# Kernel tuning notes

Measured on AMD Instinct MI355X. Metric: run time of the kernel, lower is better.

Reference implementation:

```python
import jax, jax.numpy as jnp
import numpy as np

N = 8192          # mesh vertices
E = 49152         # directed edges (avg degree 6)
M = 25            # kernel_size per pseudo-dim
DIM = 3           # pseudo-coordinate dim
K = M ** DIM      # 15625 weight matrices per layer
S = 2 ** DIM      # 8 nonzero degree-1 B-spline products per edge
LC, UC = -0.22703196, 0.36853024   # curvature range
LM, UM = 1.2585511, 1.648841       # myelin range
R = 10.0
LAYER_DIMS = [(2, 32), (32, 64), (64, 64), (64, 32), (32, 1)]


def transform(x):
    # rescale curv/myelin channels into [-R, R] with clamping (matches torch masking)
    t0 = (x[:, 0] - LC) / (UC - LC) * (2.0 * R) - R
    t1 = (x[:, 1] - LM) / (UM - LM) * (2.0 * R) - R
    return jnp.stack([jnp.clip(t0, -R, R), jnp.clip(t1, -R, R)], axis=1)


def spline_basis(pseudo):
    # open B-spline, degree 1: v in [0, M-1); 8 corner products per edge
    v = pseudo * (M - 1)
    lo = jnp.floor(v)
    f = v - lo                                                    # [E, DIM]
    lo = lo.astype(jnp.int32)
    bits = (jnp.arange(S)[:, None] >> jnp.arange(DIM)[None, :]) & 1   # [S, DIM]
    oh = bits.astype(pseudo.dtype)
    basis = jnp.prod(oh[None] * f[:, None, :] + (1.0 - oh[None]) * (1.0 - f[:, None, :]), axis=-1)  # [E, S]
    strides = (M ** jnp.arange(DIM)).astype(jnp.int32)
    wi = jnp.sum((lo[:, None, :] + bits[None]) * strides[None, None, :], axis=-1)  # [E, S] kernel indices
    return basis, wi


def spline_conv(h, src, dst, basis, wi, W, root, bias):
    xj = h[src]                                             # [E, Fin] gather
    msg = jnp.zeros((xj.shape[0], W.shape[2]), h.dtype)
    for s in range(S):                                      # fixed 8-way basis loop
        msg = msg + basis[:, s, None] * jnp.einsum('ei,eio->eo', xj, W[wi[:, s]])
    agg = jax.ops.segment_sum(msg, dst, num_segments=N)     # scatter-sum (norm=False)
    return agg + h @ root + bias


def setup_inputs() -> dict:
    key = jax.random.key(0)
    ks = jax.random.split(key, 3 + 2 * len(LAYER_DIMS))
    inp = {
        "x": jax.random.normal(ks[0], (N, 2), dtype=jnp.float32),
        "edge_index": jax.random.randint(ks[1], (2, E), 0, N),
        "pseudo": jax.random.uniform(ks[2], (E, DIM), dtype=jnp.float32),
    }
    for i, (fi, fo) in enumerate(LAYER_DIMS):
        kw, kr = ks[3 + 2 * i], ks[4 + 2 * i]
        inp[f"W{i+1}"] = jax.random.normal(kw, (K, fi, fo), dtype=jnp.float32) / np.float32(np.sqrt(fi * S))
        inp[f"root{i+1}"] = jax.random.normal(kr, (fi, fo), dtype=jnp.float32) / np.float32(np.sqrt(fi))
        inp[f"b{i+1}"] = jnp.zeros((fo,), dtype=jnp.float32)
    return inp


def reference(x, edge_index, pseudo, W1, root1, b1, W2, root2, b2, W3, root3, b3,
              W4, root4, b4, W5, root5, b5):
    src, dst = edge_index[0], edge_index[1]
    basis, wi = spline_basis(pseudo)   # shared across all 5 layers, as in the torch model
    h = transform(x)
    for W, r, b in ((W1, root1, b1), (W2, root2, b2), (W3, root3, b3),
                    (W4, root4, b4), (W5, root5, b5)):
        h = jax.nn.elu(spline_conv(h, src, dst, basis, wi, W, r, b))
    return h.reshape(-1)
```

## Files before the change

### kernel.cpp

```cpp
#include <hip/hip_runtime.h>
#include <math.h>

#define NV 8192
#define EV 49152
#define KK 15625

__device__ __forceinline__ void edge_frac(const float* __restrict__ pseudo, int e,
                                          float f[3], int lo[3]) {
#pragma unroll
    for (int j = 0; j < 3; ++j) {
        float v = pseudo[e * 3 + j] * 24.0f;
        float fl = floorf(v);
        int l = (int)fl;
        l = l < 0 ? 0 : (l > 23 ? 23 : l);
        lo[j] = l;
        f[j] = v - (float)l;
    }
}

__global__ void transform_kernel(const float* __restrict__ x, float* __restrict__ h0) {
    int n = blockIdx.x * blockDim.x + threadIdx.x;
    if (n >= NV) return;
    const float LC = -0.22703196f, UC = 0.36853024f;
    const float LM = 1.2585511f, UM = 1.648841f;
    const float R = 10.0f;
    float t0 = (x[n * 2 + 0] - LC) / (UC - LC) * (2.0f * R) - R;
    float t1 = (x[n * 2 + 1] - LM) / (UM - LM) * (2.0f * R) - R;
    h0[n * 2 + 0] = fminf(fmaxf(t0, -R), R);
    h0[n * 2 + 1] = fminf(fmaxf(t1, -R), R);
}

__global__ void hist_kernel(const float* __restrict__ pseudo, int* __restrict__ counts) {
    int e = blockIdx.x * blockDim.x + threadIdx.x;
    if (e >= EV) return;
    float f[3]; int lo[3];
    edge_frac(pseudo, e, f, lo);
#pragma unroll
    for (int s = 0; s < 8; ++s) {
        int wi = (lo[0] + (s & 1)) + 25 * (lo[1] + ((s >> 1) & 1)) + 625 * (lo[2] + ((s >> 2) & 1));
        atomicAdd(&counts[wi], 1);
    }
}

__global__ void scan_kernel(const int* __restrict__ counts, int* __restrict__ offsets,
                            int* __restrict__ cursor) {
    __shared__ int sums[256];
    const int CH = 62;
    int t = threadIdx.x;
    int base = t * CH;
    int s = 0;
    for (int i = 0; i < CH; ++i) {
        int idx = base + i;
        if (idx < KK) s += counts[idx];
    }
    sums[t] = s;
    __syncthreads();
    for (int d = 1; d < 256; d <<= 1) {
        int v = (t >= d) ? sums[t - d] : 0;
        __syncthreads();
        sums[t] += v;
        __syncthreads();
    }
    int run = (t > 0) ? sums[t - 1] : 0;
    for (int i = 0; i < CH; ++i) {
        int idx = base + i;
        if (idx < KK) {
            offsets[idx] = run;
            cursor[idx] = run;
            run += counts[idx];
        }
    }
    if (t == 255) offsets[KK] = run;
}

__global__ void scatter_kernel(const float* __restrict__ pseudo, const int* __restrict__ ei,
                               int* __restrict__ cursor,
                               int2* __restrict__ pair_sb, int* __restrict__ pair_dst) {
    int e = blockIdx.x * blockDim.x + threadIdx.x;
    if (e >= EV) return;
    float f[3]; int lo[3];
    edge_frac(pseudo, e, f, lo);
    int src = ei[e];
    int dst = ei[EV + e];
#pragma unroll
    for (int s = 0; s < 8; ++s) {
        float b = ((s & 1) ? f[0] : 1.0f - f[0]) *
                  (((s >> 1) & 1) ? f[1] : 1.0f - f[1]) *
                  (((s >> 2) & 1) ? f[2] : 1.0f - f[2]);
        int wi = (lo[0] + (s & 1)) + 25 * (lo[1] + ((s >> 1) & 1)) + 625 * (lo[2] + ((s >> 2) & 1));
        int pos = atomicAdd(&cursor[wi], 1);
        pair_sb[pos] = make_int2(src, __float_as_int(b));
        pair_dst[pos] = dst;
    }
}

template <int FIN, int FOUT>
__global__ __launch_bounds__(256) void conv_v3(
    const float* __restrict__ h, const float* __restrict__ W,
    const int* __restrict__ offsets, const int2* __restrict__ pair_sb,
    const int* __restrict__ pair_dst, float* __restrict__ agg) {
    constexpr int P = 16;
    constexpr int C4 = FIN / 4;
    constexpr int J = C4 / 4;
    constexpr int RG = 64 / FOUT;
    int w = threadIdx.x >> 6;
    int lane = threadIdx.x & 63;
    int k = blockIdx.x * 4 + w;
    if (k >= KK) return;
    int start = offsets[k];
    int n = offsets[k + 1] - start;
    if (n <= 0) return;
    int o = lane % FOUT;
    int g = lane / FOUT;
    const float* Wk = W + (size_t)k * (FIN * FOUT);
    float wreg[FIN];
#pragma unroll
    for (int i = 0; i < FIN; ++i) wreg[i] = Wk[i * FOUT + o];

    __shared__ float4 xsh[4][2][P][C4];
    int sr = lane >> 2;
    int sc = lane & 3;

    const float4* h4 = (const float4*)h;

    float4 v[J];
    auto ldpanel = [&](int p0) {
        int pp = p0 + sr;
        int2 sb = (pp < n) ? pair_sb[start + pp] : make_int2(0, 0);
        float b = __int_as_float(sb.y);
        const float4* hr = h4 + (size_t)sb.x * C4;
#pragma unroll
        for (int j = 0; j < J; ++j) {
            float4 t = hr[sc + 4 * j];
            v[j] = make_float4(t.x * b, t.y * b, t.z * b, t.w * b);
        }
    };
    auto stpanel = [&](int buf) {
#pragma unroll
        for (int j = 0; j < J; ++j) xsh[w][buf][sr][sc + 4 * j] = v[j];
    };
    auto cpanel = [&](int buf, int p0) {
        int lim = n - p0;
        if (lim > P) lim = P;
        for (int r = g; r < lim; r += RG) {
            int dst = pair_dst[start + p0 + r];
            float a0 = 0.0f, a1 = 0.0f, a2 = 0.0f, a3 = 0.0f;
#pragma unroll
            for (int i4 = 0; i4 < C4; ++i4) {
                float4 xv = xsh[w][buf][r][i4];
                a0 += xv.x * wreg[4 * i4 + 0];
                a1 += xv.y * wreg[4 * i4 + 1];
                a2 += xv.z * wreg[4 * i4 + 2];
                a3 += xv.w * wreg[4 * i4 + 3];
            }
            atomicAdd(&agg[(size_t)dst * FOUT + o], (a0 + a1) + (a2 + a3));
        }
    };

    int nP = (n + P - 1) / P;
    ldpanel(0);
    stpanel(0);
    for (int p = 0; p < nP; ++p) {
        int buf = p & 1;
        if (p + 1 < nP) ldpanel((p + 1) * P);
        cpanel(buf, p * P);
        if (p + 1 < nP) stpanel(buf ^ 1);
        __builtin_amdgcn_wave_barrier();
    }
}

__global__ __launch_bounds__(256) void conv_l1(
    const float* __restrict__ h, const float* __restrict__ W,
    const int* __restrict__ offsets, const int2* __restrict__ pair_sb,
    const int* __restrict__ pair_dst, float* __restrict__ agg) {
    int w = threadIdx.x >> 6;
    int lane = threadIdx.x & 63;
    int k = blockIdx.x * 4 + w;
    if (k >= KK) return;
    int start = offsets[k];
    int n = offsets[k + 1] - start;
    if (n <= 0) return;
    int o = lane & 31;
    int g = lane >> 5;
    const float* Wk = W + (size_t)k * 64;
    float w0 = Wk[o], w1 = Wk[32 + o];
    const float2* h2 = (const float2*)h;
    for (int r = g; r < n; r += 2) {
        int2 sb = pair_sb[start + r];
        float b = __int_as_float(sb.y);
        int dst = pair_dst[start + r];
        float2 xv = h2[sb.x];
        atomicAdd(&agg[(size_t)dst * 32 + o], b * (xv.x * w0 + xv.y * w1));
    }
}

__global__ __launch_bounds__(256) void conv_f1(
    const float* __restrict__ h, const float* __restrict__ W,
    const int* __restrict__ offsets, const int2* __restrict__ pair_sb,
    const int* __restrict__ pair_dst, float* __restrict__ agg) {
    int w = threadIdx.x >> 6;
    int lane = threadIdx.x & 63;
    int k = blockIdx.x * 4 + w;
    if (k >= KK) return;
    int start = offsets[k];
    int n = offsets[k + 1] - start;
    if (n <= 0) return;
    int i = lane & 31;
    int g = lane >> 5;
    float wk = W[(size_t)k * 32 + i];
    for (int r = g; r < n; r += 2) {
        int2 sb = pair_sb[start + r];
        float b = __int_as_float(sb.y);
        int dst = pair_dst[start + r];
        float val = h[(size_t)sb.x * 32 + i] * wk * b;
#pragma unroll
        for (int d = 16; d >= 1; d >>= 1) val += __shfl_xor(val, d, 32);
        if (i == 0) atomicAdd(&agg[dst], val);
    }
}

template <int FIN, int FOUT>
__global__ void node_kernel(const float* __restrict__ h, const float* __restrict__ agg,
                            const float* __restrict__ root, const float* __restrict__ bias,
                            float* __restrict__ hout) {
    int idx = blockIdx.x * blockDim.x + threadIdx.x;
    if (idx >= NV * FOUT) return;
    int n = idx / FOUT, o = idx % FOUT;
    float acc = agg[idx] + bias[o];
#pragma unroll
    for (int i = 0; i < FIN; ++i) acc += h[n * FIN + i] * root[i * FOUT + o];
    hout[idx] = acc > 0.0f ? acc : expm1f(acc);
}

extern "C" void kernel_launch(void* const* d_in, const int* in_sizes, int n_in,
                              void* d_out, int out_size, void* d_ws, size_t ws_size,
                              hipStream_t stream) {
    const float* x      = (const float*)d_in[0];
    const int*   ei     = (const int*)d_in[1];
    const float* pseudo = (const float*)d_in[2];
    const float* W1 = (const float*)d_in[3];
    const float* r1 = (const float*)d_in[4];
    const float* b1 = (const float*)d_in[5];
    const float* W2 = (const float*)d_in[6];
    const float* r2 = (const float*)d_in[7];
    const float* b2 = (const float*)d_in[8];
    const float* W3 = (const float*)d_in[9];
    const float* r3 = (const float*)d_in[10];
    const float* b3 = (const float*)d_in[11];
    const float* W4 = (const float*)d_in[12];
    const float* r4 = (const float*)d_in[13];
    const float* b4 = (const float*)d_in[14];
    const float* W5 = (const float*)d_in[15];
    const float* r5 = (const float*)d_in[16];
    const float* b5 = (const float*)d_in[17];

    char* ws = (char*)d_ws;
    size_t off = 0;
    auto alloc = [&](size_t bytes) {
        void* p = ws + off;
        off += (bytes + 255) & ~(size_t)255;
        return p;
    };
    int*   counts   = (int*)alloc(KK * sizeof(int));
    int*   offsets  = (int*)alloc((KK + 1) * sizeof(int));
    int*   cursor   = (int*)alloc(KK * sizeof(int));
    int2*  pair_sb  = (int2*)alloc((size_t)EV * 8 * sizeof(int2));
    int*   pair_dst = (int*)alloc((size_t)EV * 8 * sizeof(int));
    float* hA       = (float*)alloc((size_t)NV * 64 * sizeof(float));
    float* hB       = (float*)alloc((size_t)NV * 64 * sizeof(float));
    float* agg      = (float*)alloc((size_t)NV * 64 * sizeof(float));

    const int CGRID = (KK + 3) / 4;

    hipMemsetAsync(counts, 0, KK * sizeof(int), stream);
    transform_kernel<<<(NV + 255) / 256, 256, 0, stream>>>(x, hA);
    hist_kernel<<<(EV + 255) / 256, 256, 0, stream>>>(pseudo, counts);
    scan_kernel<<<1, 256, 0, stream>>>(counts, offsets, cursor);
    scatter_kernel<<<(EV + 255) / 256, 256, 0, stream>>>(pseudo, ei, cursor, pair_sb, pair_dst);

    hipMemsetAsync(agg, 0, (size_t)NV * 32 * sizeof(float), stream);
    conv_l1<<<CGRID, 256, 0, stream>>>(hA, W1, offsets, pair_sb, pair_dst, agg);
    node_kernel<2, 32><<<(NV * 32 + 255) / 256, 256, 0, stream>>>(hA, agg, r1, b1, hB);

    hipMemsetAsync(agg, 0, (size_t)NV * 64 * sizeof(float), stream);
    conv_v3<32, 64><<<CGRID, 256, 0, stream>>>(hB, W2, offsets, pair_sb, pair_dst, agg);
    node_kernel<32, 64><<<(NV * 64 + 255) / 256, 256, 0, stream>>>(hB, agg, r2, b2, hA);

    hipMemsetAsync(agg, 0, (size_t)NV * 64 * sizeof(float), stream);
    conv_v3<64, 64><<<CGRID, 256, 0, stream>>>(hA, W3, offsets, pair_sb, pair_dst, agg);
    node_kernel<64, 64><<<(NV * 64 + 255) / 256, 256, 0, stream>>>(hA, agg, r3, b3, hB);

    hipMemsetAsync(agg, 0, (size_t)NV * 32 * sizeof(float), stream);
    conv_v3<64, 32><<<CGRID, 256, 0, stream>>>(hB, W4, offsets, pair_sb, pair_dst, agg);
    node_kernel<64, 32><<<(NV * 32 + 255) / 256, 256, 0, stream>>>(hB, agg, r4, b4, hA);

    hipMemsetAsync(agg, 0, (size_t)NV * sizeof(float), stream);
    conv_f1<<<CGRID, 256, 0, stream>>>(hA, W5, offsets, pair_sb, pair_dst, agg);
    node_kernel<32, 1><<<(NV + 255) / 256, 256, 0, stream>>>(hA, agg, r5, b5, (float*)d_out);
}
```

Measured before the change: 515.9 us.

## Use split-bf16 MFMA for per-kernel-index edge matmuls in middle conv layers

Replaces the LDS double-buffered FMA conv kernel with a matrix-core version. Each wave converts its weight matrix into hi/lo bf16 pairs held in registers. For each 16-edge tile it gathers the scaled source features, splits them into bf16 hi/lo, and issues three 16x16x32 bf16 MFMAs to approximate fp32 accuracy. Results are scattered to the aggregate buffer with atomics. This removes the scalar FMA inner loop and the shared-memory staging. In exchange it adds bf16 conversion work, a higher register count, and a small precision loss, and tiles are poorly filled because there are only about 25 edges per kernel index.

```diff
diff --git a/kernel.cpp b/kernel.cpp
--- a/kernel.cpp
+++ b/kernel.cpp
@@ -4,6 +4,18 @@
 #define NV 8192
 #define EV 49152
 #define KK 15625
+
+typedef __attribute__((ext_vector_type(8))) short bf16x8;
+typedef __attribute__((ext_vector_type(4))) float f32x4;
+
+__device__ __forceinline__ unsigned short bf16rne(float x) {
+    unsigned u = __float_as_uint(x);
+    unsigned r = u + 0x7FFFu + ((u >> 16) & 1u);
+    return (unsigned short)(r >> 16);
+}
+__device__ __forceinline__ float bf16tof(unsigned short h) {
+    return __uint_as_float(((unsigned)h) << 16);
+}
 
 __device__ __forceinline__ void edge_frac(const float* __restrict__ pseudo, int e,
                                           float f[3], int lo[3]) {
@@ -95,14 +107,12 @@
 }
 
 template <int FIN, int FOUT>
-__global__ __launch_bounds__(256) void conv_v3(
+__global__ __launch_bounds__(256) void conv_mfma(
     const float* __restrict__ h, const float* __restrict__ W,
     const int* __restrict__ offsets, const int2* __restrict__ pair_sb,
     const int* __restrict__ pair_dst, float* __restrict__ agg) {
-    constexpr int P = 16;
-    constexpr int C4 = FIN / 4;
-    constexpr int J = C4 / 4;
-    constexpr int RG = 64 / FOUT;
+    constexpr int KT = FIN / 32;
+    constexpr int NT = FOUT / 16;
     int w = threadIdx.x >> 6;
     int lane = threadIdx.x & 63;
     int k = blockIdx.x * 4 + w;
@@ -110,62 +120,67 @@
     int start = offsets[k];
     int n = offsets[k + 1] - start;
     if (n <= 0) return;
-    int o = lane % FOUT;
-    int g = lane / FOUT;
+    int l15 = lane & 15;
+    int lg = lane >> 4;
+
     const float* Wk = W + (size_t)k * (FIN * FOUT);
-    float wreg[FIN];
-#pragma unroll
-    for (int i = 0; i < FIN; ++i) wreg[i] = Wk[i * FOUT + o];
-
-    __shared__ float4 xsh[4][2][P][C4];
-    int sr = lane >> 2;
-    int sc = lane & 3;
-
-    const float4* h4 = (const float4*)h;
-
-    float4 v[J];
-    auto ldpanel = [&](int p0) {
-        int pp = p0 + sr;
-        int2 sb = (pp < n) ? pair_sb[start + pp] : make_int2(0, 0);
-        float b = __int_as_float(sb.y);
-        const float4* hr = h4 + (size_t)sb.x * C4;
-#pragma unroll
-        for (int j = 0; j < J; ++j) {
-            float4 t = hr[sc + 4 * j];
-            v[j] = make_float4(t.x * b, t.y * b, t.z * b, t.w * b);
+    bf16x8 Bh[NT][KT], Bl[NT][KT];
+#pragma unroll
+    for (int n0 = 0; n0 < NT; ++n0)
+#pragma unroll
+        for (int k0 = 0; k0 < KT; ++k0)
+#pragma unroll
+            for (int i = 0; i < 8; ++i) {
+                float wv = Wk[(size_t)(k0 * 32 + lg * 8 + i) * FOUT + n0 * 16 + l15];
+                unsigned short hi = bf16rne(wv);
+                unsigned short lo = bf16rne(wv - bf16tof(hi));
+                Bh[n0][k0][i] = (short)hi;
+                Bl[n0][k0][i] = (short)lo;
+            }
+
+    for (int m0 = 0; m0 < n; m0 += 16) {
+        int ra = m0 + l15;
+        bool va = ra < n;
+        int2 sb = pair_sb[start + (va ? ra : 0)];
+        float b = va ? __int_as_float(sb.y) : 0.0f;
+        const float* xr = h + (size_t)sb.x * FIN + lg * 8;
+
+        f32x4 acc[NT];
+#pragma unroll
+        for (int n0 = 0; n0 < NT; ++n0) acc[n0] = (f32x4){0.f, 0.f, 0.f, 0.f};
+
+#pragma unroll
+        for (int k0 = 0; k0 < KT; ++k0) {
+            float4 v0 = *(const float4*)(xr + k0 * 32);
+            float4 v1 = *(const float4*)(xr + k0 * 32 + 4);
+            float xv[8] = {v0.x * b, v0.y * b, v0.z * b, v0.w * b,
+                           v1.x * b, v1.y * b, v1.z * b, v1.w * b};
+            bf16x8 Ah, Al;
+#pragma unroll
+            for (int i = 0; i < 8; ++i) {
+                unsigned short hi = bf16rne(xv[i]);
+                unsigned short lo = bf16rne(xv[i] - bf16tof(hi));
+                Ah[i] = (short)hi;
+                Al[i] = (short)lo;
+            }
+#pragma unroll
+            for (int n0 = 0; n0 < NT; ++n0) {
+                acc[n0] = __builtin_amdgcn_mfma_f32_16x16x32_bf16(Ah, Bh[n0][k0], acc[n0], 0, 0, 0);
+                acc[n0] = __builtin_amdgcn_mfma_f32_16x16x32_bf16(Ah, Bl[n0][k0], acc[n0], 0, 0, 0);
+                acc[n0] = __builtin_amdgcn_mfma_f32_16x16x32_bf16(Al, Bh[n0][k0], acc[n0], 0, 0, 0);
+            }
         }
-    };
-    auto stpanel = [&](int buf) {
-#pragma unroll
-        for (int j = 0; j < J; ++j) xsh[w][buf][sr][sc + 4 * j] = v[j];
-    };
-    auto cpanel = [&](int buf, int p0) {
-        int lim = n - p0;
-        if (lim > P) lim = P;
-        for (int r = g; r < lim; r += RG) {
-            int dst = pair_dst[start + p0 + r];
-            float a0 = 0.0f, a1 = 0.0f, a2 = 0.0f, a3 = 0.0f;
-#pragma unroll
-            for (int i4 = 0; i4 < C4; ++i4) {
-                float4 xv = xsh[w][buf][r][i4];
-                a0 += xv.x * wreg[4 * i4 + 0];
-                a1 += xv.y * wreg[4 * i4 + 1];
-                a2 += xv.z * wreg[4 * i4 + 2];
-                a3 += xv.w * wreg[4 * i4 + 3];
+
+#pragma unroll
+        for (int j = 0; j < 4; ++j) {
+            int rm = m0 + lg * 4 + j;
+            if (rm < n) {
+                int d = pair_dst[start + rm];
+#pragma unroll
+                for (int n0 = 0; n0 < NT; ++n0)
+                    atomicAdd(&agg[(size_t)d * FOUT + n0 * 16 + l15], acc[n0][j]);
             }
-            atomicAdd(&agg[(size_t)dst * FOUT + o], (a0 + a1) + (a2 + a3));
         }
-    };
-
-    int nP = (n + P - 1) / P;
-    ldpanel(0);
-    stpanel(0);
-    for (int p = 0; p < nP; ++p) {
-        int buf = p & 1;
-        if (p + 1 < nP) ldpanel((p + 1) * P);
-        cpanel(buf, p * P);
-        if (p + 1 < nP) stpanel(buf ^ 1);
-        __builtin_amdgcn_wave_barrier();
     }
 }
 
@@ -283,15 +298,15 @@
     node_kernel<2, 32><<<(NV * 32 + 255) / 256, 256, 0, stream>>>(hA, agg, r1, b1, hB);
 
     hipMemsetAsync(agg, 0, (size_t)NV * 64 * sizeof(float), stream);
-    conv_v3<32, 64><<<CGRID, 256, 0, stream>>>(hB, W2, offsets, pair_sb, pair_dst, agg);
+    conv_mfma<32, 64><<<CGRID, 256, 0, stream>>>(hB, W2, offsets, pair_sb, pair_dst, agg);
     node_kernel<32, 64><<<(NV * 64 + 255) / 256, 256, 0, stream>>>(hB, agg, r2, b2, hA);
 
     hipMemsetAsync(agg, 0, (size_t)NV * 64 * sizeof(float), stream);
-    conv_v3<64, 64><<<CGRID, 256, 0, stream>>>(hA, W3, offsets, pair_sb, pair_dst, agg);
+    conv_mfma<64, 64><<<CGRID, 256, 0, stream>>>(hA, W3, offsets, pair_sb, pair_dst, agg);
     node_kernel<64, 64><<<(NV * 64 + 255) / 256, 256, 0, stream>>>(hA, agg, r3, b3, hB);
 
     hipMemsetAsync(agg, 0, (size_t)NV * 32 * sizeof(float), stream);
-    conv_v3<64, 32><<<CGRID, 256, 0, stream>>>(hB, W4, offsets, pair_sb, pair_dst, agg);
+    conv_mfma<64, 32><<<CGRID, 256, 0, stream>>>(hB, W4, offsets, pair_sb, pair_dst, agg);
     node_kernel<64, 32><<<(NV * 32 + 255) / 256, 256, 0, stream>>>(hB, agg, r4, b4, hA);
 
     hipMemsetAsync(agg, 0, (size_t)NV * sizeof(float), stream);
```

Result: no change. 509.9 us (-1.2%).
